# Optimization experiments

Measured on AMD Instinct MI355X. Metric: run time of the kernel, lower is better.

The kernel has to match this reference:

```python
import jax, jax.numpy as jnp
import numpy as np

BATCH = 16384
N_FEAT = 2048
SWAP_PROB = 0.1


def setup_inputs() -> dict:
    key = jax.random.key(0)
    k_x, k_mask, k_perm = jax.random.split(key, 3)
    x = jax.random.normal(k_x, (BATCH, N_FEAT), dtype=jnp.float32)
    # swap_mask[i, j] = True with prob swap_prob (matches torch.rand(...) < swap_prob)
    swap_mask = jax.random.uniform(k_mask, (BATCH, N_FEAT)) < SWAP_PROB
    # per-row random permutation (matches torch.randperm per batch row),
    # vectorized as argsort of iid uniforms
    perm = jnp.argsort(jax.random.uniform(k_perm, (BATCH, N_FEAT)), axis=1).astype(jnp.int32)
    return {"x": x, "swap_mask": swap_mask, "perm": perm}


def reference(x, swap_mask, perm):
    # x[i, swap_mask[i]] = x[i, perm[i][swap_mask[i]]]  (vectorized over rows)
    swapped = jnp.take_along_axis(x, perm, axis=1)  # [B, F]
    return jnp.where(swap_mask, swapped, x)
```

## Files before the change

kernel.cpp:

```cpp
#include <hip/hip_runtime.h>

#define NFEAT 2048
#define BATCH 16384
#define WPB   4

__global__ __launch_bounds__(256) void swap_corrupt_kernel(
    const float* __restrict__ x,
    const int*   __restrict__ mask,
    const int*   __restrict__ perm,
    float*       __restrict__ out)
{
    __shared__ float rows[WPB][NFEAT];

    const int t    = threadIdx.x;
    const int w    = t >> 6;
    const int lane = t & 63;
    const int r    = blockIdx.x * WPB + w;
    const size_t base = (size_t)r * NFEAT;

    auto* lrow = (__attribute__((address_space(3))) float*)(&rows[w][0]);
    const auto* gx = (const __attribute__((address_space(1))) float*)(x + base);
#pragma unroll
    for (int c = 0; c < 8; ++c) {
        __builtin_amdgcn_global_load_lds(
            (const __attribute__((address_space(1))) void*)(gx + c * 256 + lane * 4),
            (__attribute__((address_space(3))) void*)(lrow + c * 256),
            16, 0, 0);
    }

    const int4* __restrict__ m4 = (const int4*)(mask + base);
    const int4* __restrict__ p4 = (const int4*)(perm + base);
    int4 m[8], p[8];
#pragma unroll
    for (int c = 0; c < 8; ++c) {
        m[c] = m4[c * 64 + lane];
        p[c] = p4[c * 64 + lane];
    }

    asm volatile("s_waitcnt vmcnt(0)" ::: "memory");

    const float* row = &rows[w][0];
    float4* __restrict__ o4 = (float4*)(out + base);
#pragma unroll
    for (int c = 0; c < 8; ++c) {
        const int e0 = c * 256 + lane * 4;
        float4 o;
        o.x = row[m[c].x ? p[c].x : e0    ];
        o.y = row[m[c].y ? p[c].y : e0 + 1];
        o.z = row[m[c].z ? p[c].z : e0 + 2];
        o.w = row[m[c].w ? p[c].w : e0 + 3];
        o4[c * 64 + lane] = o;
    }
}

extern "C" void kernel_launch(void* const* d_in, const int* in_sizes, int n_in,
                              void* d_out, int out_size, void* d_ws, size_t ws_size,
                              hipStream_t stream) {
    const float* x    = (const float*)d_in[0];
    const int*   mask = (const int*)d_in[1];
    const int*   perm = (const int*)d_in[2];
    float*       out  = (float*)d_out;

    swap_corrupt_kernel<<<dim3(BATCH / WPB), dim3(256), 0, stream>>>(x, mask, perm, out);
}
```

Baseline: 388.1 us.

## Process one row per block with shared LDS row and nontemporal stores

Changes the mapping from one row per wavefront (four rows per block) to one row per 256-thread block, so all four waves cooperatively stage the row into LDS and sync with a block barrier. Each thread now handles two float4 chunks instead of eight. Non-swapped values are read as vectorized float4 from LDS, and only masked elements do a scalar gather. Outputs go out through nontemporal stores. This aims to raise occupancy, cut LDS per block and register pressure, and avoid polluting the cache with output, at the cost of a block-wide barrier and four times as many blocks.

```diff
diff --git a/kernel.cpp b/kernel.cpp
--- a/kernel.cpp
+++ b/kernel.cpp
@@ -2,7 +2,8 @@
 
 #define NFEAT 2048
 #define BATCH 16384
-#define WPB   4
+
+typedef float  v4f __attribute__((ext_vector_type(4)));
 
 __global__ __launch_bounds__(256) void swap_corrupt_kernel(
     const float* __restrict__ x,
@@ -10,46 +11,49 @@
     const int*   __restrict__ perm,
     float*       __restrict__ out)
 {
-    __shared__ float rows[WPB][NFEAT];
+    __shared__ float row[NFEAT];
 
     const int t    = threadIdx.x;
+    const int lane = t & 63;
     const int w    = t >> 6;
-    const int lane = t & 63;
-    const int r    = blockIdx.x * WPB + w;
-    const size_t base = (size_t)r * NFEAT;
+    const size_t base = (size_t)blockIdx.x * NFEAT;
 
-    auto* lrow = (__attribute__((address_space(3))) float*)(&rows[w][0]);
-    const auto* gx = (const __attribute__((address_space(1))) float*)(x + base);
+    const auto* gx   = (const __attribute__((address_space(1))) float*)(x + base);
+    auto*       lrow = (__attribute__((address_space(3))) float*)row;
 #pragma unroll
-    for (int c = 0; c < 8; ++c) {
+    for (int c = 0; c < 2; ++c) {
+        const int off = w * 512 + c * 256;
         __builtin_amdgcn_global_load_lds(
-            (const __attribute__((address_space(1))) void*)(gx + c * 256 + lane * 4),
-            (__attribute__((address_space(3))) void*)(lrow + c * 256),
+            (const __attribute__((address_space(1))) void*)(gx + off + lane * 4),
+            (__attribute__((address_space(3))) void*)(lrow + off),
             16, 0, 0);
     }
 
     const int4* __restrict__ m4 = (const int4*)(mask + base);
     const int4* __restrict__ p4 = (const int4*)(perm + base);
-    int4 m[8], p[8];
-#pragma unroll
-    for (int c = 0; c < 8; ++c) {
-        m[c] = m4[c * 64 + lane];
-        p[c] = p4[c * 64 + lane];
+    int4 m0 = m4[t], m1 = m4[t + 256];
+    int4 p0 = p4[t], p1 = p4[t + 256];
+
+    __syncthreads();
+
+    v4f* __restrict__ o4 = (v4f*)(out + base);
+    {
+        float4 a = ((const float4*)row)[t];
+        v4f o;
+        o.x = m0.x ? row[p0.x] : a.x;
+        o.y = m0.y ? row[p0.y] : a.y;
+        o.z = m0.z ? row[p0.z] : a.z;
+        o.w = m0.w ? row[p0.w] : a.w;
+        __builtin_nontemporal_store(o, &o4[t]);
     }
-
-    asm volatile("s_waitcnt vmcnt(0)" ::: "memory");
-
-    const float* row = &rows[w][0];
-    float4* __restrict__ o4 = (float4*)(out + base);
-#pragma unroll
-    for (int c = 0; c < 8; ++c) {
-        const int e0 = c * 256 + lane * 4;
-        float4 o;
-        o.x = row[m[c].x ? p[c].x : e0    ];
-        o.y = row[m[c].y ? p[c].y : e0 + 1];
-        o.z = row[m[c].z ? p[c].z : e0 + 2];
-        o.w = row[m[c].w ? p[c].w : e0 + 3];
-        o4[c * 64 + lane] = o;
+    {
+        float4 b = ((const float4*)row)[t + 256];
+        v4f o;
+        o.x = m1.x ? row[p1.x] : b.x;
+        o.y = m1.y ? row[p1.y] : b.y;
+        o.z = m1.z ? row[p1.z] : b.z;
+        o.w = m1.w ? row[p1.w] : b.w;
+        __builtin_nontemporal_store(o, &o4[t + 256]);
     }
 }
 
@@ -61,5 +65,5 @@
     const int*   perm = (const int*)d_in[2];
     float*       out  = (float*)d_out;
 
-    swap_corrupt_kernel<<<dim3(BATCH / WPB), dim3(256), 0, stream>>>(x, mask, perm, out);
+    swap_corrupt_kernel<<<dim3(BATCH), dim3(256), 0, stream>>>(x, mask, perm, out);
 }
```

Measured after the change: 388.5 us. Within noise of the previous version (+0.1%).
